# Performance work log

Hardware: AMD Instinct MI355X
Metric: run time of the kernel (lower is better)

Reference implementation:

```python
import jax, jax.numpy as jnp
import numpy as np

TEMPERATURE = 0.5
EPSILON = 1e-9


def _l2_normalize(x, eps=1e-12):
    # matches torch F.normalize(p=2, dim=-1): x / max(||x||, eps)
    n = jnp.linalg.norm(x, axis=-1, keepdims=True)
    return x / jnp.maximum(n, eps)


def setup_inputs() -> dict:
    key = jax.random.key(0)
    k1, k2, k3 = jax.random.split(key, 3)
    N, D, V = 8192, 128, 3
    H_consensus = jax.random.normal(k1, (N, D), dtype=jnp.float32)
    S_similarity = jax.random.uniform(k2, (N, N), dtype=jnp.float32)
    H_views = jax.random.normal(k3, (V, N, D), dtype=jnp.float32)
    return {"H_consensus": H_consensus, "S_similarity": S_similarity, "H_views": H_views}


def reference(H_consensus, S_similarity, H_views):
    N = H_consensus.shape[0]
    V = H_views.shape[0]
    Hc = _l2_normalize(H_consensus)            # [N, D]
    Hv = _l2_normalize(H_views)                # [V, N, D]
    sim = jnp.einsum('nd,vmd->vnm', Hc, Hv)    # [V, N, N]
    positive = jnp.diagonal(sim, axis1=1, axis2=2) / TEMPERATURE  # [V, N]
    weights = 1.0 - S_similarity               # [N, N], broadcast over V
    denom = jnp.sum(weights * jnp.exp(sim / TEMPERATURE), axis=-1)  # [V, N]
    denom = jnp.maximum(denom, EPSILON)
    loss = -(positive - jnp.log(denom))        # [V, N]
    return jnp.sum(loss) / (N * V)
```

## Files before the change

kernel.cpp:

```cpp
#include <hip/hip_runtime.h>
#include <hip/hip_bf16.h>

constexpr int kN = 8192;
constexpr int kD = 128;
constexpr int kV = 3;
constexpr int kNV = kV * kN;
constexpr int kNChunk = 512;
constexpr int kNTile = 32;
constexpr int kIters = kNChunk / kNTile;
constexpr int kAccStride = 529;
constexpr float kLn2 = 0.6931471805599453f;
constexpr float kScaleHc = 2.885390081777927f;

typedef __attribute__((ext_vector_type(8))) short bf16x8;
typedef __attribute__((ext_vector_type(4))) float floatx4;

#if __has_builtin(__builtin_amdgcn_exp2f)
#define EXP2F(x) __builtin_amdgcn_exp2f(x)
#else
#define EXP2F(x) exp2f(x)
#endif

__device__ __forceinline__ unsigned pack_bf16(float a, float b) {
    unsigned ua = __float_as_uint(a);
    unsigned ub = __float_as_uint(b);
    ua = (ua + 0x7FFFu + ((ua >> 16) & 1u)) >> 16;
    ub = (ub + 0x7FFFu + ((ub >> 16) & 1u)) >> 16;
    return ua | (ub << 16);
}

__device__ __forceinline__ float quad_sum(float p) {
    float t = p;
    asm("v_permlane16_swap_b32 %0, %1" : "+v"(p), "+v"(t));
    p += t;
    t = p;
    asm("v_permlane32_swap_b32 %0, %1" : "+v"(p), "+v"(t));
    return p + t;
}

__global__ void k_normalize(const float* __restrict__ Hc, const float* __restrict__ Hv,
                            unsigned* __restrict__ HcB, unsigned* __restrict__ HvB) {
    int row  = (blockIdx.x * blockDim.x + threadIdx.x) >> 6;
    int lane = threadIdx.x & 63;
    const float* src;
    unsigned* dst;
    float extra;
    if (row < kN) { src = Hc + (size_t)row * kD; dst = HcB + (size_t)row * (kD / 2); extra = kScaleHc; }
    else {
        int r = row - kN;
        src = Hv + (size_t)r * kD; dst = HvB + (size_t)r * (kD / 2); extra = 1.0f;
    }
    float2 x = ((const float2*)src)[lane];
    float ss = x.x * x.x + x.y * x.y;
    ss += __shfl_xor(ss, 1);  ss += __shfl_xor(ss, 2);  ss += __shfl_xor(ss, 4);
    ss += __shfl_xor(ss, 8);  ss += __shfl_xor(ss, 16); ss += __shfl_xor(ss, 32);
    float inv = extra * rsqrtf(fmaxf(ss, 1e-24f));
    dst[lane] = pack_bf16(x.x * inv, x.y * inv);
}

__global__ void k_positive(const unsigned* __restrict__ HcB, const unsigned* __restrict__ HvB,
                           float* __restrict__ pos_partial) {
    int row  = (blockIdx.x * blockDim.x + threadIdx.x) >> 6;
    int lane = threadIdx.x & 63;
    int w    = threadIdx.x >> 6;
    int n    = row & (kN - 1);
    unsigned a = HcB[(size_t)n * (kD / 2) + lane];
    unsigned b = HvB[(size_t)row * (kD / 2) + lane];
    float dot = __uint_as_float(a << 16) * __uint_as_float(b << 16)
              + __uint_as_float(a & 0xFFFF0000u) * __uint_as_float(b & 0xFFFF0000u);
    dot += __shfl_xor(dot, 1);  dot += __shfl_xor(dot, 2);  dot += __shfl_xor(dot, 4);
    dot += __shfl_xor(dot, 8);  dot += __shfl_xor(dot, 16); dot += __shfl_xor(dot, 32);
    __shared__ float acc4[4];
    if (lane == 0) acc4[w] = dot;
    __syncthreads();
    if (threadIdx.x == 0)
        atomicAdd(&pos_partial[blockIdx.x & 255], acc4[0] + acc4[1] + acc4[2] + acc4[3]);
}

__launch_bounds__(256, 3)
__global__ void k_main(const unsigned* __restrict__ HcB, const unsigned* __restrict__ HvB,
                       const float* __restrict__ S, float* __restrict__ denom) {
    __shared__ short Htile[2][kNTile * 136];
    __shared__ float accum[kV * kAccStride];

    const int tid  = threadIdx.x;
    const int w    = tid >> 6;
    const int lane = tid & 63;
    const int col  = lane & 15;
    const int quad = lane >> 4;
    const int m0b  = blockIdx.x * 64;
    const int m0w  = m0b + w * 16;
    const int nbase = blockIdx.y * kNChunk;
    const int sr = tid >> 4;
    const int sc = tid & 15;

    for (int i = tid; i < kV * kAccStride; i += 256) accum[i] = 0.f;

    bf16x8 afrag[kV][4];
#pragma unroll
    for (int v = 0; v < kV; ++v) {
        const short* rowp = (const short*)HvB + ((size_t)(v * kN + m0w + col)) * kD;
#pragma unroll
        for (int kk = 0; kk < 4; ++kk)
            afrag[v][kk] = *(const bf16x8*)(rowp + kk * 32 + quad * 8);
    }

    const short* hc = (const short*)HcB;
    const float* Sp = S + (size_t)(nbase + col) * kN + m0b + (w << 4) + (quad << 2);

    {
        float4 ha = *(const float4*)(hc + (size_t)(nbase + sr) * kD + sc * 8);
        float4 hb = *(const float4*)(hc + (size_t)(nbase + sr + 16) * kD + sc * 8);
        *(float4*)&Htile[0][sr * 136 + sc * 8]        = ha;
        *(float4*)&Htile[0][(sr + 16) * 136 + sc * 8] = hb;
    }
    float4 s0 = *(const float4*)(Sp);
    float4 s1 = *(const float4*)(Sp + (size_t)16 * kN);
    __syncthreads();

    for (int it = 0; it < kIters; ++it) {
        int itn = (it + 1 < kIters) ? it + 1 : it;
        int n0n = nbase + itn * kNTile;
        float4 ha  = *(const float4*)(hc + (size_t)(n0n + sr) * kD + sc * 8);
        float4 hb  = *(const float4*)(hc + (size_t)(n0n + sr + 16) * kD + sc * 8);
        float4 s0n = *(const float4*)(Sp + (size_t)(itn * 32) * kN);
        float4 s1n = *(const float4*)(Sp + (size_t)(itn * 32 + 16) * kN);

        const int cur = it & 1;
#pragma unroll
        for (int sub = 0; sub < 2; ++sub) {
            const int nrow = sub * 16 + col;
            bf16x8 bfrag[4];
#pragma unroll
            for (int kk = 0; kk < 4; ++kk)
                bfrag[kk] = *(const bf16x8*)&Htile[cur][nrow * 136 + kk * 32 + quad * 8];
            float4 s4 = sub ? s1 : s0;

            floatx4 acc0 = {0.f,0.f,0.f,0.f}, acc1 = {0.f,0.f,0.f,0.f}, acc2 = {0.f,0.f,0.f,0.f};
#pragma unroll
            for (int kk = 0; kk < 4; ++kk) {
                acc0 = __builtin_amdgcn_mfma_f32_16x16x32_bf16(afrag[0][kk], bfrag[kk], acc0, 0, 0, 0);
                acc1 = __builtin_amdgcn_mfma_f32_16x16x32_bf16(afrag[1][kk], bfrag[kk], acc1, 0, 0, 0);
                acc2 = __builtin_amdgcn_mfma_f32_16x16x32_bf16(afrag[2][kk], bfrag[kk], acc2, 0, 0, 0);
            }
            float w0 = 1.f - s4.x, w1 = 1.f - s4.y, w2 = 1.f - s4.z, w3 = 1.f - s4.w;
            float p0 = w0 * EXP2F(acc0[0]) + w1 * EXP2F(acc0[1]) + w2 * EXP2F(acc0[2]) + w3 * EXP2F(acc0[3]);
            float p1 = w0 * EXP2F(acc1[0]) + w1 * EXP2F(acc1[1]) + w2 * EXP2F(acc1[2]) + w3 * EXP2F(acc1[3]);
            float p2 = w0 * EXP2F(acc2[0]) + w1 * EXP2F(acc2[1]) + w2 * EXP2F(acc2[2]) + w3 * EXP2F(acc2[3]);
            p0 = quad_sum(p0);
            p1 = quad_sum(p1);
            p2 = quad_sum(p2);
            float val = (quad == 0) ? p0 : ((quad == 1) ? p1 : p2);
            if (quad < 3)
                atomicAdd(&accum[quad * kAccStride + it * kNTile + sub * 16 + col], val);
        }

        s0 = s0n; s1 = s1n;
        const int nxt = cur ^ 1;
        *(float4*)&Htile[nxt][sr * 136 + sc * 8]        = ha;
        *(float4*)&Htile[nxt][(sr + 16) * 136 + sc * 8] = hb;
        __syncthreads();
    }

    for (int i = tid; i < kV * kNChunk; i += 256) {
        int v = i >> 9, c = i & (kNChunk - 1);
        atomicAdd(&denom[(size_t)v * kN + nbase + c], accum[v * kAccStride + c]);
    }
}

__global__ void k_final(const float* __restrict__ denom, const float* __restrict__ pos_partial,
                        float* __restrict__ out) {
    int idx  = blockIdx.x * 256 + threadIdx.x;
    int lane = threadIdx.x & 63;
    int w    = threadIdx.x >> 6;
    float val = logf(fmaxf(denom[idx], 1e-9f));
    if (blockIdx.x == 0) val -= pos_partial[threadIdx.x] * kLn2;
    val += __shfl_xor(val, 1);  val += __shfl_xor(val, 2);  val += __shfl_xor(val, 4);
    val += __shfl_xor(val, 8);  val += __shfl_xor(val, 16); val += __shfl_xor(val, 32);
    __shared__ float acc4[4];
    if (lane == 0) acc4[w] = val;
    __syncthreads();
    if (threadIdx.x == 0)
        atomicAdd(out, (acc4[0] + acc4[1] + acc4[2] + acc4[3]) * (1.0f / kNV));
}

extern "C" void kernel_launch(void* const* d_in, const int* in_sizes, int n_in,
                              void* d_out, int out_size, void* d_ws, size_t ws_size,
                              hipStream_t stream) {
    const float* Hc = (const float*)d_in[0];
    const float* S  = (const float*)d_in[1];
    const float* Hv = (const float*)d_in[2];

    unsigned* HcB  = (unsigned*)d_ws;
    unsigned* HvB  = HcB + (size_t)kN * (kD / 2);
    float*    den  = (float*)(HvB + (size_t)kV * kN * (kD / 2));
    float*    posp = den + kNV;
    float*    outF = (float*)d_out;

    hipMemsetAsync(den, 0, ((size_t)kNV + 256) * sizeof(float), stream);
    hipMemsetAsync(outF, 0, sizeof(float), stream);

    k_normalize<<<dim3((kN + kV * kN) / 4), 256, 0, stream>>>(Hc, Hv, HcB, HvB);
    k_positive<<<dim3(kNV / 4), 256, 0, stream>>>(HcB, HvB, posp);
    k_main<<<dim3(kN / 64, kN / kNChunk), dim3(256), 0, stream>>>(HcB, HvB, S, den);
    k_final<<<dim3(kNV / 256), dim3(256), 0, stream>>>(den, posp, outF);
}
```

Baseline: 412.7 us.

## Load Hc fragments directly from global, drop LDS staging and per-iteration barriers

Each wave now loads its B-operand fragments of the normalized consensus rows straight from global memory into registers, one iteration ahead, instead of staging them cooperatively in a double-buffered LDS tile with a __syncthreads per iteration. The S weights are prefetched two iterations ahead. Per-row results go into per-wave LDS accumulators with plain stores rather than shared atomics, and the waves' partials are summed at the end. Occupancy hint rises to 4 blocks. This trades redundant global/L2 reads of Hc across the four waves for removing barriers and LDS atomics.

```diff
diff --git a/kernel.cpp b/kernel.cpp
--- a/kernel.cpp
+++ b/kernel.cpp
@@ -6,8 +6,8 @@
 constexpr int kV = 3;
 constexpr int kNV = kV * kN;
 constexpr int kNChunk = 512;
-constexpr int kNTile = 32;
-constexpr int kIters = kNChunk / kNTile;
+constexpr int kRows = 16;
+constexpr int kIters = kNChunk / kRows;
 constexpr int kAccStride = 529;
 constexpr float kLn2 = 0.6931471805599453f;
 constexpr float kScaleHc = 2.885390081777927f;
@@ -77,11 +77,10 @@
         atomicAdd(&pos_partial[blockIdx.x & 255], acc4[0] + acc4[1] + acc4[2] + acc4[3]);
 }
 
-__launch_bounds__(256, 3)
+__launch_bounds__(256, 4)
 __global__ void k_main(const unsigned* __restrict__ HcB, const unsigned* __restrict__ HvB,
                        const float* __restrict__ S, float* __restrict__ denom) {
-    __shared__ short Htile[2][kNTile * 136];
-    __shared__ float accum[kV * kAccStride];
+    __shared__ float accum[4 * kV * kAccStride];
 
     const int tid  = threadIdx.x;
     const int w    = tid >> 6;
@@ -91,10 +90,6 @@
     const int m0b  = blockIdx.x * 64;
     const int m0w  = m0b + w * 16;
     const int nbase = blockIdx.y * kNChunk;
-    const int sr = tid >> 4;
-    const int sc = tid & 15;
-
-    for (int i = tid; i < kV * kAccStride; i += 256) accum[i] = 0.f;
 
     bf16x8 afrag[kV][4];
 #pragma unroll
@@ -106,65 +101,56 @@
     }
 
     const short* hc = (const short*)HcB;
+    const short* hp = hc + (size_t)(nbase + col) * kD + (quad << 3);
     const float* Sp = S + (size_t)(nbase + col) * kN + m0b + (w << 4) + (quad << 2);
 
-    {
-        float4 ha = *(const float4*)(hc + (size_t)(nbase + sr) * kD + sc * 8);
-        float4 hb = *(const float4*)(hc + (size_t)(nbase + sr + 16) * kD + sc * 8);
-        *(float4*)&Htile[0][sr * 136 + sc * 8]        = ha;
-        *(float4*)&Htile[0][(sr + 16) * 136 + sc * 8] = hb;
-    }
-    float4 s0 = *(const float4*)(Sp);
-    float4 s1 = *(const float4*)(Sp + (size_t)16 * kN);
-    __syncthreads();
+    bf16x8 bfA[4];
+#pragma unroll
+    for (int kk = 0; kk < 4; ++kk) bfA[kk] = *(const bf16x8*)(hp + kk * 32);
+    float4 sCur = *(const float4*)(Sp);
+    float4 sNxt = *(const float4*)(Sp + (size_t)kRows * kN);
 
+#pragma unroll 4
     for (int it = 0; it < kIters; ++it) {
-        int itn = (it + 1 < kIters) ? it + 1 : it;
-        int n0n = nbase + itn * kNTile;
-        float4 ha  = *(const float4*)(hc + (size_t)(n0n + sr) * kD + sc * 8);
-        float4 hb  = *(const float4*)(hc + (size_t)(n0n + sr + 16) * kD + sc * 8);
-        float4 s0n = *(const float4*)(Sp + (size_t)(itn * 32) * kN);
-        float4 s1n = *(const float4*)(Sp + (size_t)(itn * 32 + 16) * kN);
+        const int itn = (it + 1 < kIters) ? it + 1 : it;
+        const int it2 = (it + 2 < kIters) ? it + 2 : it;
+        bf16x8 bfN[4];
+#pragma unroll
+        for (int kk = 0; kk < 4; ++kk)
+            bfN[kk] = *(const bf16x8*)(hp + (size_t)itn * kRows * kD + kk * 32);
+        float4 sN2 = *(const float4*)(Sp + (size_t)it2 * kRows * kN);
 
-        const int cur = it & 1;
+        floatx4 acc0 = {0.f,0.f,0.f,0.f}, acc1 = {0.f,0.f,0.f,0.f}, acc2 = {0.f,0.f,0.f,0.f};
 #pragma unroll
-        for (int sub = 0; sub < 2; ++sub) {
-            const int nrow = sub * 16 + col;
-            bf16x8 bfrag[4];
+        for (int kk = 0; kk < 4; ++kk) {
+            acc0 = __builtin_amdgcn_mfma_f32_16x16x32_bf16(afrag[0][kk], bfA[kk], acc0, 0, 0, 0);
+            acc1 = __builtin_amdgcn_mfma_f32_16x16x32_bf16(afrag[1][kk], bfA[kk], acc1, 0, 0, 0);
+            acc2 = __builtin_amdgcn_mfma_f32_16x16x32_bf16(afrag[2][kk], bfA[kk], acc2, 0, 0, 0);
+        }
+        float w0 = 1.f - sCur.x, w1 = 1.f - sCur.y, w2 = 1.f - sCur.z, w3 = 1.f - sCur.w;
+        float p0 = w0 * EXP2F(acc0[0]) + w1 * EXP2F(acc0[1]) + w2 * EXP2F(acc0[2]) + w3 * EXP2F(acc0[3]);
+        float p1 = w0 * EXP2F(acc1[0]) + w1 * EXP2F(acc1[1]) + w2 * EXP2F(acc1[2]) + w3 * EXP2F(acc1[3]);
+        float p2 = w0 * EXP2F(acc2[0]) + w1 * EXP2F(acc2[1]) + w2 * EXP2F(acc2[2]) + w3 * EXP2F(acc2[3]);
+        p0 = quad_sum(p0);
+        p1 = quad_sum(p1);
+        p2 = quad_sum(p2);
+        float val = (quad == 0) ? p0 : ((quad == 1) ? p1 : p2);
+        if (quad < 3)
+            accum[(w * kV + quad) * kAccStride + it * kRows + col] = val;
+
 #pragma unroll
-            for (int kk = 0; kk < 4; ++kk)
-                bfrag[kk] = *(const bf16x8*)&Htile[cur][nrow * 136 + kk * 32 + quad * 8];
-            float4 s4 = sub ? s1 : s0;
-
-            floatx4 acc0 = {0.f,0.f,0.f,0.f}, acc1 = {0.f,0.f,0.f,0.f}, acc2 = {0.f,0.f,0.f,0.f};
-#pragma unroll
-            for (int kk = 0; kk < 4; ++kk) {
-                acc0 = __builtin_amdgcn_mfma_f32_16x16x32_bf16(afrag[0][kk], bfrag[kk], acc0, 0, 0, 0);
-                acc1 = __builtin_amdgcn_mfma_f32_16x16x32_bf16(afrag[1][kk], bfrag[kk], acc1, 0, 0, 0);
-                acc2 = __builtin_amdgcn_mfma_f32_16x16x32_bf16(afrag[2][kk], bfrag[kk], acc2, 0, 0, 0);
-            }
-            float w0 = 1.f - s4.x, w1 = 1.f - s4.y, w2 = 1.f - s4.z, w3 = 1.f - s4.w;
-            float p0 = w0 * EXP2F(acc0[0]) + w1 * EXP2F(acc0[1]) + w2 * EXP2F(acc0[2]) + w3 * EXP2F(acc0[3]);
-            float p1 = w0 * EXP2F(acc1[0]) + w1 * EXP2F(acc1[1]) + w2 * EXP2F(acc1[2]) + w3 * EXP2F(acc1[3]);
-            float p2 = w0 * EXP2F(acc2[0]) + w1 * EXP2F(acc2[1]) + w2 * EXP2F(acc2[2]) + w3 * EXP2F(acc2[3]);
-            p0 = quad_sum(p0);
-            p1 = quad_sum(p1);
-            p2 = quad_sum(p2);
-            float val = (quad == 0) ? p0 : ((quad == 1) ? p1 : p2);
-            if (quad < 3)
-                atomicAdd(&accum[quad * kAccStride + it * kNTile + sub * 16 + col], val);
-        }
-
-        s0 = s0n; s1 = s1n;
-        const int nxt = cur ^ 1;
-        *(float4*)&Htile[nxt][sr * 136 + sc * 8]        = ha;
-        *(float4*)&Htile[nxt][(sr + 16) * 136 + sc * 8] = hb;
-        __syncthreads();
+        for (int kk = 0; kk < 4; ++kk) bfA[kk] = bfN[kk];
+        sCur = sNxt; sNxt = sN2;
     }
 
+    __syncthreads();
     for (int i = tid; i < kV * kNChunk; i += 256) {
         int v = i >> 9, c = i & (kNChunk - 1);
-        atomicAdd(&denom[(size_t)v * kN + nbase + c], accum[v * kAccStride + c]);
+        float sum = accum[(0 * kV + v) * kAccStride + c]
+                  + accum[(1 * kV + v) * kAccStride + c]
+                  + accum[(2 * kV + v) * kAccStride + c]
+                  + accum[(3 * kV + v) * kAccStride + c];
+        atomicAdd(&denom[(size_t)v * kN + nbase + c], sum);
     }
 }
 
```

New measurement: 472.6 us. +14.5%, slower.
